# Kernel optimization log

Measured on AMD Instinct MI355X. Metric: run time of the kernel, lower is better.

The kernel has to match this reference:

```python
import jax, jax.numpy as jnp
import numpy as np

B, N, H, T = 128, 512, 128, 32


def setup_inputs() -> dict:
    key = jax.random.key(0)
    ks = jax.random.split(key, 6)
    s = 0.05  # small init scale keeps softmax logits sane
    return {
        "encoder_outputs": jax.random.normal(ks[0], (B, N, H), jnp.float32),
        "W_ih": jax.random.normal(ks[1], (4 * H, H), jnp.float32) * s,
        "W_hh": jax.random.normal(ks[2], (4 * H, H), jnp.float32) * s,
        "b_ih": jnp.zeros((4 * H,), jnp.float32),
        "b_hh": jnp.zeros((4 * H,), jnp.float32),
        "W1": jax.random.normal(ks[3], (H, H), jnp.float32) * s,
        "W2": jax.random.normal(ks[4], (H, H), jnp.float32) * s,
        "v": jax.random.normal(ks[5], (H,), jnp.float32) * s,
        "decode_steps": T,
    }


def reference(encoder_outputs, W_ih, W_hh, b_ih, b_hh, W1, W2, v, decode_steps):
    b, n, h = encoder_outputs.shape
    dtype = encoder_outputs.dtype
    # W1(encoder_outputs) is loop-invariant: hoist it (same math as the torch loop)
    enc_trans = jnp.einsum("bnh,kh->bnk", encoder_outputs, W1)  # [B,n,H]

    dec0 = encoder_outputs.mean(axis=1)  # [B,H]
    hx0 = jnp.zeros((b, h), dtype)
    cx0 = jnp.zeros((b, h), dtype)
    mask0 = jnp.zeros((b, n), bool)
    key0 = jax.random.key(42)
    rows = jnp.arange(b)

    def step(carry, _):
        dec_input, hx, cx, mask, key = carry
        # torch.nn.LSTMCell: gates ordered i, f, g, o
        gates = dec_input @ W_ih.T + b_ih + hx @ W_hh.T + b_hh  # [B,4H]
        i, f, g, o = jnp.split(gates, 4, axis=-1)
        i = jax.nn.sigmoid(i)
        f = jax.nn.sigmoid(f)
        g = jnp.tanh(g)
        o = jax.nn.sigmoid(o)
        cx_new = f * cx + i * g
        hx_new = o * jnp.tanh(cx_new)
        # additive attention scores
        dec_trans = hx_new @ W2.T  # [B,H]
        scores = jnp.einsum("bnh,h->bn", jnp.tanh(enc_trans + dec_trans[:, None, :]), v)
        scores = jnp.where(mask, -jnp.inf, scores)  # masked_fill(-inf)
        # sample next node (torch.multinomial on softmax == categorical on logits)
        key, sub = jax.random.split(key)
        idx = jax.random.categorical(sub, scores, axis=-1)  # [B]
        probs = jax.nn.softmax(scores, axis=-1)
        sel_log_prob = jnp.log(jnp.take_along_axis(probs, idx[:, None], axis=1)[:, 0] + 1e-9)
        mask_new = mask.at[rows, idx].set(True)
        dec_next = jnp.take_along_axis(encoder_outputs, idx[:, None, None], axis=1)[:, 0]  # [B,H]
        return (dec_next, hx_new, cx_new, mask_new, key), (idx, sel_log_prob)

    _, (tours, log_probs) = jax.lax.scan(
        step, (dec0, hx0, cx0, mask0, key0), xs=None, length=decode_steps
    )
    return tours.T, log_probs.T  # [B,T], [B,T]
```

## Files before the change

kernel.cpp:

```cpp
#include <hip/hip_runtime.h>
#include <cstdint>
#include <cstddef>


constexpr int B = 128, N = 512, H = 128, T = 32;
constexpr int G4 = 4 * H;
constexpr float TINYF = 1.17549435e-38f;

__host__ __device__ inline uint32_t rotl32(uint32_t v, int d) {
  return (v << d) | (v >> (32 - d));
}

__host__ __device__ inline void tf2x32(uint32_t k0, uint32_t k1,
                                       uint32_t x0, uint32_t x1,
                                       uint32_t& o0, uint32_t& o1) {
  uint32_t ks2 = k0 ^ k1 ^ 0x1BD11BDAu;
  x0 += k0; x1 += k1;
#define TF_R(r) x0 += x1; x1 = rotl32(x1, (r)); x1 ^= x0;
  TF_R(13) TF_R(15) TF_R(26) TF_R(6)
  x0 += k1; x1 += ks2 + 1u;
  TF_R(17) TF_R(29) TF_R(16) TF_R(24)
  x0 += ks2; x1 += k0 + 2u;
  TF_R(13) TF_R(15) TF_R(26) TF_R(6)
  x0 += k0; x1 += k1 + 3u;
  TF_R(17) TF_R(29) TF_R(16) TF_R(24)
  x0 += k1; x1 += ks2 + 4u;
  TF_R(13) TF_R(15) TF_R(26) TF_R(6)
  x0 += ks2; x1 += k0 + 5u;
#undef TF_R
  o0 = x0; o1 = x1;
}

struct KeyArgs { uint32_t k[2 * T]; };

static KeyArgs make_subkeys() {
  KeyArgs ka;
  uint32_t k0 = 0u, k1 = 42u;
  for (int t = 0; t < T; ++t) {
    uint32_t n0, n1, s0, s1;
    tf2x32(k0, k1, 0u, 0u, n0, n1);
    tf2x32(k0, k1, 0u, 1u, s0, s1);
    ka.k[2 * t] = s0; ka.k[2 * t + 1] = s1;
    k0 = n0; k1 = n1;
  }
  return ka;
}

__device__ inline uint32_t gumbel_bits(uint32_t sk0, uint32_t sk1, int i) {
  uint32_t o0, o1;
  tf2x32(sk0, sk1, 0u, (uint32_t)i, o0, o1);
  return o0 ^ o1;
}

__device__ inline float fast_tanh(float x) {
  float cx = fminf(9.0f, fmaxf(-9.0f, x));
  float t = __expf(2.0f * cx);
  return (t - 1.0f) * __builtin_amdgcn_rcpf(t + 1.0f);
}

__global__ void k_transpose(const float* __restrict__ Wih, const float* __restrict__ Whh,
                            const float* __restrict__ W2, const float* __restrict__ W1,
                            float* __restrict__ WihT, float* __restrict__ WhhT,
                            float* __restrict__ W2T, float* __restrict__ W1T) {
  int i = blockIdx.x * blockDim.x + threadIdx.x;
  if (i < H * G4) {
    int h = i >> 9, j = i & (G4 - 1);
    WihT[i] = Wih[j * H + h];
  } else if (i < 2 * H * G4) {
    int q = i - H * G4; int h = q >> 9, j = q & (G4 - 1);
    WhhT[q] = Whh[j * H + h];
  } else if (i < 2 * H * G4 + H * H) {
    int q = i - 2 * H * G4; int h = q >> 7, k = q & (H - 1);
    W2T[q] = W2[k * H + h];
  } else if (i < 2 * H * G4 + 2 * H * H) {
    int q = i - 2 * H * G4 - H * H; int h = q >> 7, k = q & (H - 1);
    W1T[q] = W1[k * H + h];
  }
}

__global__ __launch_bounds__(256) void k_enc_trans(const float* __restrict__ enc,
                                                   const float* __restrict__ W1T,
                                                   float* __restrict__ encT2) {
  __shared__ __align__(16) float es[16 * 128];
  int blk = blockIdx.x;
  int b = blk >> 5;
  int n0 = (blk & 31) << 4;
  const float* src = enc + ((size_t)b * N + n0) * H;
  for (int i = threadIdx.x; i < 16 * 128; i += 256) es[i] = src[i];
  __syncthreads();
  int k = threadIdx.x & 127, ng = threadIdx.x >> 7;
  float acc[8] = {0.f, 0.f, 0.f, 0.f, 0.f, 0.f, 0.f, 0.f};
  for (int h = 0; h < H; h += 4) {
    float w0 = W1T[(h + 0) * H + k];
    float w1 = W1T[(h + 1) * H + k];
    float w2 = W1T[(h + 2) * H + k];
    float w3 = W1T[(h + 3) * H + k];
#pragma unroll
    for (int j = 0; j < 8; ++j) {
      const float4 e = *(const float4*)&es[(ng * 8 + j) * 128 + h];
      acc[j] += w0 * e.x + w1 * e.y + w2 * e.z + w3 * e.w;
    }
  }
  float* dst = encT2 + (size_t)b * H * N + (size_t)k * N + n0 + ng * 8;
  ((float4*)dst)[0] = make_float4(acc[0], acc[1], acc[2], acc[3]);
  ((float4*)dst)[1] = make_float4(acc[4], acc[5], acc[6], acc[7]);
}

#define REP16(M) M(0) M(1) M(2) M(3) M(4) M(5) M(6) M(7) \
                 M(8) M(9) M(10) M(11) M(12) M(13) M(14) M(15)

__global__ __launch_bounds__(512)
__attribute__((amdgpu_waves_per_eu(2, 2))) void k_decode(
    const float* __restrict__ enc, const float* __restrict__ encT2,
    const float* __restrict__ WihT, const float* __restrict__ WhhT,
    const float* __restrict__ W2T,
    const float* __restrict__ bih, const float* __restrict__ bhh,
    const float* __restrict__ v,
    KeyArgs keys, float* __restrict__ out) {
  __shared__ __align__(16) float xs[H];
  __shared__ __align__(16) float hs[H];
  __shared__ __align__(16) float cs[H];
  __shared__ __align__(16) float dt[H];
  __shared__ __align__(16) float vv[H];
  __shared__ __align__(16) float bsum[G4];
  __shared__ float pg[G4];
  __shared__ float pdt[4][H];
  __shared__ float sc[N];
  __shared__ float wr_z[8], wr_m[8], wr_s[8];
  __shared__ int wr_i[8];
  __shared__ float s_smax;
  __shared__ int s_idx;

  extern __shared__ __align__(16) float e_lds[];

  const int tid = threadIdx.x;
  const int b = blockIdx.x;
  const int lane = tid & 63;
  const int wave = tid >> 6;

  const float* ep = encT2 + (size_t)b * (H * N) + tid;
#define ERLD(i) float4 er##i = make_float4(ep[(size_t)(4*i+0) * N], \
                                           ep[(size_t)(4*i+1) * N], \
                                           ep[(size_t)(4*i+2) * N], \
                                           ep[(size_t)(4*i+3) * N]);
  REP16(ERLD)
#undef ERLD

  {
    const float4* src4 = (const float4*)(encT2 + (size_t)b * (H * N) + (size_t)64 * N);
    float4* dst4 = (float4*)e_lds;
#pragma unroll
    for (int i = 0; i < 16; ++i) dst4[tid + i * 512] = src4[tid + i * 512];
  }

  {
    int h = tid & 127, part = tid >> 7;
    float s = 0.f;
    const float* p = enc + ((size_t)b * N + part * 128) * H + h;
#pragma unroll 8
    for (int n = 0; n < 128; ++n) s += p[(size_t)n * H];
    pdt[part][h] = s;
    bsum[tid] = bih[tid] + bhh[tid];
  }
  if (tid < 128) { hs[tid] = 0.f; cs[tid] = 0.f; vv[tid] = v[tid]; }
  __syncthreads();
  if (tid < 128)
    xs[tid] = (pdt[0][tid] + pdt[1][tid] + pdt[2][tid] + pdt[3][tid]) * (1.0f / N);
  bool masked = false;
  __syncthreads();

  for (int t = 0; t < T; ++t) {
    {
      const float* wi = WihT + tid;
      const float* wh = WhhT + tid;
      float a0x = 0.f, a0h = 0.f, a1x = 0.f, a1h = 0.f;
#pragma unroll 8
      for (int h = 0; h < 64; h += 4) {
        const float4 xv = *(const float4*)&xs[h];
        a0x += wi[(size_t)(h + 0) * G4] * xv.x;
        a0x += wi[(size_t)(h + 1) * G4] * xv.y;
        a0x += wi[(size_t)(h + 2) * G4] * xv.z;
        a0x += wi[(size_t)(h + 3) * G4] * xv.w;
        const float4 hv = *(const float4*)&hs[h];
        a0h += wh[(size_t)(h + 0) * G4] * hv.x;
        a0h += wh[(size_t)(h + 1) * G4] * hv.y;
        a0h += wh[(size_t)(h + 2) * G4] * hv.z;
        a0h += wh[(size_t)(h + 3) * G4] * hv.w;
      }
#pragma unroll 8
      for (int h = 64; h < 128; h += 4) {
        const float4 xv = *(const float4*)&xs[h];
        a1x += wi[(size_t)(h + 0) * G4] * xv.x;
        a1x += wi[(size_t)(h + 1) * G4] * xv.y;
        a1x += wi[(size_t)(h + 2) * G4] * xv.z;
        a1x += wi[(size_t)(h + 3) * G4] * xv.w;
        const float4 hv = *(const float4*)&hs[h];
        a1h += wh[(size_t)(h + 0) * G4] * hv.x;
        a1h += wh[(size_t)(h + 1) * G4] * hv.y;
        a1h += wh[(size_t)(h + 2) * G4] * hv.z;
        a1h += wh[(size_t)(h + 3) * G4] * hv.w;
      }
      pg[tid] = (a0x + a0h) + (a1x + a1h);
    }
    __syncthreads();
    if (tid < 128) {
      float gi = pg[tid] + bsum[tid];
      float gf = pg[H + tid] + bsum[H + tid];
      float gg = pg[2 * H + tid] + bsum[2 * H + tid];
      float go = pg[3 * H + tid] + bsum[3 * H + tid];
      gi = 1.0f / (1.0f + expf(-gi));
      gf = 1.0f / (1.0f + expf(-gf));
      gg = tanhf(gg);
      go = 1.0f / (1.0f + expf(-go));
      float c = gf * cs[tid] + gi * gg;
      cs[tid] = c;
      hs[tid] = go * tanhf(c);
    }
    __syncthreads();
    {
      int k = tid & 127, part = tid >> 7;
      const float* w2 = W2T + (size_t)(part * 32) * H + k;
      const int hbp = part * 32;
      float a = 0.f;
#pragma unroll 8
      for (int h = 0; h < 32; h += 4) {
        const float4 hv = *(const float4*)&hs[hbp + h];
        a += w2[(size_t)(h + 0) * H] * hv.x;
        a += w2[(size_t)(h + 1) * H] * hv.y;
        a += w2[(size_t)(h + 2) * H] * hv.z;
        a += w2[(size_t)(h + 3) * H] * hv.w;
      }
      pdt[part][k] = a;
    }
    __syncthreads();
    if (tid < 128) dt[tid] = pdt[0][tid] + pdt[1][tid] + pdt[2][tid] + pdt[3][tid];
    __syncthreads();
    float s_score;
    {
      float a0 = 0.f, a1 = 0.f;
#define P4A(i) { const float4 dv = *(const float4*)&dt[4 * i];              \
                 const float4 vw = *(const float4*)&vv[4 * i];              \
                 a0 += vw.x * fast_tanh(er##i.x + dv.x);                    \
                 a1 += vw.y * fast_tanh(er##i.y + dv.y);                    \
                 a0 += vw.z * fast_tanh(er##i.z + dv.z);                    \
                 a1 += vw.w * fast_tanh(er##i.w + dv.w); }
      REP16(P4A)
#undef P4A
      float b0 = 0.f, b1 = 0.f;
#pragma unroll
      for (int k4 = 0; k4 < 64; k4 += 4) {
        const float e0 = e_lds[(k4 + 0) * N + tid];
        const float e1 = e_lds[(k4 + 1) * N + tid];
        const float e2 = e_lds[(k4 + 2) * N + tid];
        const float e3 = e_lds[(k4 + 3) * N + tid];
        const float4 dv = *(const float4*)&dt[64 + k4];
        const float4 vw = *(const float4*)&vv[64 + k4];
        b0 += vw.x * fast_tanh(e0 + dv.x);
        b1 += vw.y * fast_tanh(e1 + dv.y);
        b0 += vw.z * fast_tanh(e2 + dv.z);
        b1 += vw.w * fast_tanh(e3 + dv.w);
      }
      s_score = (a0 + a1) + (b0 + b1);
    }
    float s = masked ? -INFINITY : s_score;
    sc[tid] = s;
    {
      uint32_t bits = gumbel_bits(keys.k[2 * t], keys.k[2 * t + 1], b * N + tid);
      float f = __uint_as_float((bits >> 9) | 0x3f800000u) - 1.0f;
      float u = fmaxf(TINYF, f + TINYF);
      float g = -logf(-logf(u));
      float z = s + g;
      int zi = tid;
      float m = s;
#pragma unroll
      for (int d = 32; d >= 1; d >>= 1) {
        float oz = __shfl_xor(z, d);
        int oi = __shfl_xor(zi, d);
        float om = __shfl_xor(m, d);
        if (oz > z || (oz == z && oi < zi)) { z = oz; zi = oi; }
        m = fmaxf(m, om);
      }
      if (lane == 0) { wr_z[wave] = z; wr_i[wave] = zi; wr_m[wave] = m; }
    }
    __syncthreads();
    if (tid == 0) {
      float bz = wr_z[0]; int bi = wr_i[0]; float bm = wr_m[0];
#pragma unroll
      for (int w = 1; w < 8; ++w) {
        if (wr_z[w] > bz || (wr_z[w] == bz && wr_i[w] < bi)) { bz = wr_z[w]; bi = wr_i[w]; }
        bm = fmaxf(bm, wr_m[w]);
      }
      s_idx = bi; s_smax = bm;
    }
    __syncthreads();
    {
      float xnew = 0.f;
      if (tid < 128) xnew = enc[((size_t)b * N + s_idx) * H + tid];
      float e = expf(s - s_smax);
#pragma unroll
      for (int d = 32; d >= 1; d >>= 1) e += __shfl_xor(e, d);
      if (lane == 0) wr_s[wave] = e;
      if (tid == s_idx) masked = true;
      if (tid < 128) xs[tid] = xnew;
    }
    __syncthreads();
    if (tid == 0) {
      float sum = wr_s[0] + wr_s[1] + wr_s[2] + wr_s[3]
                + wr_s[4] + wr_s[5] + wr_s[6] + wr_s[7];
      float p = expf(sc[s_idx] - s_smax) / sum;
      out[(size_t)b * T + t] = (float)s_idx;
      out[(size_t)B * T + (size_t)b * T + t] = logf(p + 1e-9f);
    }
    __syncthreads();
  }
}

extern "C" void kernel_launch(void* const* d_in, const int* in_sizes, int n_in,
                              void* d_out, int out_size, void* d_ws, size_t ws_size,
                              hipStream_t stream) {
  (void)in_sizes; (void)n_in; (void)out_size; (void)ws_size;
  const float* enc = (const float*)d_in[0];
  const float* Wih = (const float*)d_in[1];
  const float* Whh = (const float*)d_in[2];
  const float* bih = (const float*)d_in[3];
  const float* bhh = (const float*)d_in[4];
  const float* W1  = (const float*)d_in[5];
  const float* W2  = (const float*)d_in[6];
  const float* v   = (const float*)d_in[7];
  float* out = (float*)d_out;
  float* ws = (float*)d_ws;

  float* WihT  = ws;
  float* WhhT  = ws + 65536;
  float* W2T   = ws + 131072;
  float* W1T   = ws + 147456;
  float* encT2 = ws + 163840;

  KeyArgs keys = make_subkeys();

  static bool lds_attr_set = false;
  if (!lds_attr_set) {
    (void)hipFuncSetAttribute(reinterpret_cast<const void*>(k_decode),
                              hipFuncAttributeMaxDynamicSharedMemorySize, 131072);
    lds_attr_set = true;
  }

  k_transpose<<<640, 256, 0, stream>>>(Wih, Whh, W2, W1, WihT, WhhT, W2T, W1T);
  k_enc_trans<<<B * N / 16, 256, 0, stream>>>(enc, W1T, encT2);
  k_decode<<<B, 512, 131072, stream>>>(enc, encT2, WihT, WhhT, W2T, bih, bhh, v, keys, out);
}
```

Before: 590.3 us.

## Interleave weight layout for float4 loads and remove per-step barriers in decode loop

The weight transposes now interleave groups of four input rows, so the LSTM gate and W2 matvecs read float4 vectors from global memory instead of scalar strided loads. Each decode step also drops two block barriers. Every thread now redundantly reduces the per-wave argmax and max, rather than thread 0 writing them to shared memory. The output write is deferred into the start of the next step, with a final write after the loop. Risks are the race-safety of the deferred read of wr_s and sc, and added redundant work per thread.

```diff
diff --git a/kernel.cpp b/kernel.cpp
--- a/kernel.cpp
+++ b/kernel.cpp
@@ -64,14 +64,16 @@
                             float* __restrict__ W2T, float* __restrict__ W1T) {
   int i = blockIdx.x * blockDim.x + threadIdx.x;
   if (i < H * G4) {
-    int h = i >> 9, j = i & (G4 - 1);
-    WihT[i] = Wih[j * H + h];
+    int c = i & 3, j = (i >> 2) & 511, h4 = i >> 11;
+    WihT[i] = Wih[j * H + h4 * 4 + c];
   } else if (i < 2 * H * G4) {
-    int q = i - H * G4; int h = q >> 9, j = q & (G4 - 1);
-    WhhT[q] = Whh[j * H + h];
+    int q = i - H * G4;
+    int c = q & 3, j = (q >> 2) & 511, h4 = q >> 11;
+    WhhT[q] = Whh[j * H + h4 * 4 + c];
   } else if (i < 2 * H * G4 + H * H) {
-    int q = i - 2 * H * G4; int h = q >> 7, k = q & (H - 1);
-    W2T[q] = W2[k * H + h];
+    int q = i - 2 * H * G4;
+    int c = q & 3, k = (q >> 2) & 127, h4 = q >> 9;
+    W2T[q] = W2[k * H + h4 * 4 + c];
   } else if (i < 2 * H * G4 + 2 * H * H) {
     int q = i - 2 * H * G4 - H * H; int h = q >> 7, k = q & (H - 1);
     W1T[q] = W1[k * H + h];
@@ -128,8 +130,6 @@
   __shared__ float sc[N];
   __shared__ float wr_z[8], wr_m[8], wr_s[8];
   __shared__ int wr_i[8];
-  __shared__ float s_smax;
-  __shared__ int s_idx;
 
   extern __shared__ __align__(16) float e_lds[];
 
@@ -167,38 +167,39 @@
   if (tid < 128)
     xs[tid] = (pdt[0][tid] + pdt[1][tid] + pdt[2][tid] + pdt[3][tid]) * (1.0f / N);
   bool masked = false;
+  int sidx_r = 0;
+  float smax_r = 0.f;
   __syncthreads();
 
   for (int t = 0; t < T; ++t) {
     {
-      const float* wi = WihT + tid;
-      const float* wh = WhhT + tid;
+      if (tid == 0 && t > 0) {
+        float sum = wr_s[0] + wr_s[1] + wr_s[2] + wr_s[3]
+                  + wr_s[4] + wr_s[5] + wr_s[6] + wr_s[7];
+        float p = expf(sc[sidx_r] - smax_r) / sum;
+        out[(size_t)b * T + (t - 1)] = (float)sidx_r;
+        out[(size_t)B * T + (size_t)b * T + (t - 1)] = logf(p + 1e-9f);
+      }
+      const float4* wi4 = (const float4*)WihT + tid;
+      const float4* wh4 = (const float4*)WhhT + tid;
       float a0x = 0.f, a0h = 0.f, a1x = 0.f, a1h = 0.f;
-#pragma unroll 8
-      for (int h = 0; h < 64; h += 4) {
-        const float4 xv = *(const float4*)&xs[h];
-        a0x += wi[(size_t)(h + 0) * G4] * xv.x;
-        a0x += wi[(size_t)(h + 1) * G4] * xv.y;
-        a0x += wi[(size_t)(h + 2) * G4] * xv.z;
-        a0x += wi[(size_t)(h + 3) * G4] * xv.w;
-        const float4 hv = *(const float4*)&hs[h];
-        a0h += wh[(size_t)(h + 0) * G4] * hv.x;
-        a0h += wh[(size_t)(h + 1) * G4] * hv.y;
-        a0h += wh[(size_t)(h + 2) * G4] * hv.z;
-        a0h += wh[(size_t)(h + 3) * G4] * hv.w;
-      }
-#pragma unroll 8
-      for (int h = 64; h < 128; h += 4) {
-        const float4 xv = *(const float4*)&xs[h];
-        a1x += wi[(size_t)(h + 0) * G4] * xv.x;
-        a1x += wi[(size_t)(h + 1) * G4] * xv.y;
-        a1x += wi[(size_t)(h + 2) * G4] * xv.z;
-        a1x += wi[(size_t)(h + 3) * G4] * xv.w;
-        const float4 hv = *(const float4*)&hs[h];
-        a1h += wh[(size_t)(h + 0) * G4] * hv.x;
-        a1h += wh[(size_t)(h + 1) * G4] * hv.y;
-        a1h += wh[(size_t)(h + 2) * G4] * hv.z;
-        a1h += wh[(size_t)(h + 3) * G4] * hv.w;
+#pragma unroll
+      for (int h4 = 0; h4 < 16; ++h4) {
+        const float4 w = wi4[(size_t)h4 * 512];
+        const float4 u = wh4[(size_t)h4 * 512];
+        const float4 xv = *(const float4*)&xs[h4 * 4];
+        const float4 hv = *(const float4*)&hs[h4 * 4];
+        a0x += w.x * xv.x; a0x += w.y * xv.y; a0x += w.z * xv.z; a0x += w.w * xv.w;
+        a0h += u.x * hv.x; a0h += u.y * hv.y; a0h += u.z * hv.z; a0h += u.w * hv.w;
+      }
+#pragma unroll
+      for (int h4 = 16; h4 < 32; ++h4) {
+        const float4 w = wi4[(size_t)h4 * 512];
+        const float4 u = wh4[(size_t)h4 * 512];
+        const float4 xv = *(const float4*)&xs[h4 * 4];
+        const float4 hv = *(const float4*)&hs[h4 * 4];
+        a1x += w.x * xv.x; a1x += w.y * xv.y; a1x += w.z * xv.z; a1x += w.w * xv.w;
+        a1h += u.x * hv.x; a1h += u.y * hv.y; a1h += u.z * hv.z; a1h += u.w * hv.w;
       }
       pg[tid] = (a0x + a0h) + (a1x + a1h);
     }
@@ -219,23 +220,20 @@
     __syncthreads();
     {
       int k = tid & 127, part = tid >> 7;
-      const float* w2 = W2T + (size_t)(part * 32) * H + k;
-      const int hbp = part * 32;
+      const float4* w24 = (const float4*)W2T + (size_t)(part * 8) * H + k;
       float a = 0.f;
-#pragma unroll 8
-      for (int h = 0; h < 32; h += 4) {
-        const float4 hv = *(const float4*)&hs[hbp + h];
-        a += w2[(size_t)(h + 0) * H] * hv.x;
-        a += w2[(size_t)(h + 1) * H] * hv.y;
-        a += w2[(size_t)(h + 2) * H] * hv.z;
-        a += w2[(size_t)(h + 3) * H] * hv.w;
+#pragma unroll
+      for (int q = 0; q < 8; ++q) {
+        const float4 u = w24[(size_t)q * H];
+        const float4 hv = *(const float4*)&hs[part * 32 + q * 4];
+        a += u.x * hv.x; a += u.y * hv.y; a += u.z * hv.z; a += u.w * hv.w;
       }
       pdt[part][k] = a;
     }
     __syncthreads();
     if (tid < 128) dt[tid] = pdt[0][tid] + pdt[1][tid] + pdt[2][tid] + pdt[3][tid];
     __syncthreads();
-    float s_score;
+    float s;
     {
       float a0 = 0.f, a1 = 0.f;
 #define P4A(i) { const float4 dv = *(const float4*)&dt[4 * i];              \
@@ -260,11 +258,9 @@
         b0 += vw.z * fast_tanh(e2 + dv.z);
         b1 += vw.w * fast_tanh(e3 + dv.w);
       }
-      s_score = (a0 + a1) + (b0 + b1);
-    }
-    float s = masked ? -INFINITY : s_score;
-    sc[tid] = s;
-    {
+      const float s_score = (a0 + a1) + (b0 + b1);
+      s = masked ? -INFINITY : s_score;
+      sc[tid] = s;
       uint32_t bits = gumbel_bits(keys.k[2 * t], keys.k[2 * t + 1], b * N + tid);
       float f = __uint_as_float((bits >> 9) | 0x3f800000u) - 1.0f;
       float u = fmaxf(TINYF, f + TINYF);
@@ -283,35 +279,31 @@
       if (lane == 0) { wr_z[wave] = z; wr_i[wave] = zi; wr_m[wave] = m; }
     }
     __syncthreads();
-    if (tid == 0) {
+    {
       float bz = wr_z[0]; int bi = wr_i[0]; float bm = wr_m[0];
 #pragma unroll
       for (int w = 1; w < 8; ++w) {
         if (wr_z[w] > bz || (wr_z[w] == bz && wr_i[w] < bi)) { bz = wr_z[w]; bi = wr_i[w]; }
         bm = fmaxf(bm, wr_m[w]);
       }
-      s_idx = bi; s_smax = bm;
-    }
-    __syncthreads();
-    {
+      sidx_r = bi; smax_r = bm;
       float xnew = 0.f;
-      if (tid < 128) xnew = enc[((size_t)b * N + s_idx) * H + tid];
-      float e = expf(s - s_smax);
+      if (tid < 128) xnew = enc[((size_t)b * N + bi) * H + tid];
+      float e = expf(s - bm);
 #pragma unroll
       for (int d = 32; d >= 1; d >>= 1) e += __shfl_xor(e, d);
       if (lane == 0) wr_s[wave] = e;
-      if (tid == s_idx) masked = true;
+      if (tid == bi) masked = true;
       if (tid < 128) xs[tid] = xnew;
     }
     __syncthreads();
-    if (tid == 0) {
-      float sum = wr_s[0] + wr_s[1] + wr_s[2] + wr_s[3]
-                + wr_s[4] + wr_s[5] + wr_s[6] + wr_s[7];
-      float p = expf(sc[s_idx] - s_smax) / sum;
-      out[(size_t)b * T + t] = (float)s_idx;
-      out[(size_t)B * T + (size_t)b * T + t] = logf(p + 1e-9f);
-    }
-    __syncthreads();
+  }
+  if (tid == 0) {
+    float sum = wr_s[0] + wr_s[1] + wr_s[2] + wr_s[3]
+              + wr_s[4] + wr_s[5] + wr_s[6] + wr_s[7];
+    float p = expf(sc[sidx_r] - smax_r) / sum;
+    out[(size_t)b * T + (T - 1)] = (float)sidx_r;
+    out[(size_t)B * T + (size_t)b * T + (T - 1)] = logf(p + 1e-9f);
   }
 }
 
@@ -347,5 +339,6 @@
 
   k_transpose<<<640, 256, 0, stream>>>(Wih, Whh, W2, W1, WihT, WhhT, W2T, W1T);
   k_enc_trans<<<B * N / 16, 256, 0, stream>>>(enc, W1T, encT2);
-  k_decode<<<B, 512, 131072, stream>>>(enc, encT2, WihT, WhhT, W2T, bih, bhh, v, keys, out);
-}
+  k_decode<<<B, 512, 131072, stream>>>(enc, encT2, WihT, WhhT, W2T,
+                                       bih, bhh, v, keys, out);
+}
```

New measurement: 1.649 ms. 179% more time.
